# Performance work log

Hardware: AMD Instinct MI355X
Metric: run time of the kernel (lower is better)

Reference implementation:

```python
import jax, jax.numpy as jnp
import numpy as np

NUM_ENT = 50000
DIM = 128
NUM_REL = 1000  # num_rel * 2 (inverse relations)
E = 300000
SLOPE = 0.2      # args.leaky_relu_w
BN_EPS = 1e-5


def _leaky(x):
    return jax.nn.leaky_relu(x, SLOPE)


def _l2norm(x):
    n = jnp.linalg.norm(x, axis=-1, keepdims=True)
    return x / jnp.maximum(n, 1e-12)


def _batchnorm(x):
    # BatchNorm1d, training mode, fresh gamma=1/beta=0
    m = x.mean(axis=0)
    v = x.var(axis=0)
    return (x - m) / jnp.sqrt(v + BN_EPS)


def _propagate(i, j, etype, rel, x, watt, aatt, gcn, norm, num_ent):
    # gather -> relation-aware transform (opn='mult') -> attention -> scatter-add
    trans = x[j] * rel[etype]                       # [E, D]
    comb = jnp.concatenate([x[i], trans], axis=1)   # [E, 2D]
    score = (_leaky(comb @ watt) @ aatt)[:, 0]      # [E]
    # scatter softmax of attention score over destination nodes
    m = jax.ops.segment_max(score, i, num_segments=num_ent)
    m = jnp.where(jnp.isfinite(m), m, 0.0)
    e = jnp.exp(score - m[i])
    s = jax.ops.segment_sum(e, i, num_segments=num_ent)
    alpha = e / (s[i] + 1e-16)
    msg = (trans @ gcn) * alpha[:, None]
    if norm is not None:
        msg = msg * norm[:, None]
    return jax.ops.segment_sum(msg, i, num_segments=num_ent)


def _conv(ent, rel_in, edge_index, edge_type, w1, w2, gcn, loop_rel, watt, aatt):
    # RelationalAwareLayer.forward
    num_ent = ent.shape[0]
    rel = jnp.concatenate([rel_in, loop_rel], axis=0)
    rel = _leaky(rel @ w1) @ w2
    row, col = edge_index[0], edge_index[1]
    deg = jax.ops.segment_sum(jnp.ones((row.shape[0],), jnp.float32), row, num_segments=num_ent)
    dinv = jnp.where(deg > 0, deg ** -0.5, 0.0)
    norm = dinv[row]
    msg_n = _propagate(row, col, edge_type, rel, ent, watt, aatt, gcn, norm, num_ent)
    idx = jnp.arange(num_ent)
    loop_t = jnp.full((num_ent,), rel.shape[0] - 1)
    msg_s = _propagate(idx, idx, loop_t, rel, ent, watt, aatt, gcn, None, num_ent)
    return jnp.tanh(_batchnorm((msg_n + msg_s) / 2.0))


def setup_inputs() -> dict:
    key = jax.random.key(0)
    ks = jax.random.split(key, 24)
    g = lambda k, s: jax.random.normal(k, s, dtype=jnp.float32) * 0.05
    return {
        'edge_index': jax.random.randint(ks[0], (2, E), 0, NUM_ENT),
        'edge_type': jax.random.randint(ks[1], (E,), 0, NUM_REL),
        'ent_info_att': g(ks[2], (NUM_ENT, DIM)),
        'ent_completion_att': g(ks[3], (NUM_ENT, DIM)),
        'rel_completion_att': g(ks[4], (NUM_REL, DIM)),
        'rel_info_att': g(ks[5], (NUM_REL, DIM)),
        'align_linear1_1': g(ks[6], (2 * DIM, DIM)),
        'align_linear1_2': g(ks[7], (DIM, DIM)),
        'align_linear2_1': g(ks[8], (2 * DIM, DIM)),
        'align_linear2_2': g(ks[9], (DIM, DIM)),
        'rel_linear11': g(ks[10], (DIM, DIM)),
        'rel_linear12': g(ks[11], (DIM, DIM)),
        'rel_linear11_align': g(ks[12], (DIM, DIM)),
        'rel_linear12_align': g(ks[13], (DIM, DIM)),
        'all_linear_comp': g(ks[14], (3 * DIM, DIM)),
        # stacked per-layer conv params: [conv1_align, conv1_completion, conv2_align]
        'conv_w1': g(ks[15], (3, DIM, DIM)),
        'conv_w2': g(ks[16], (3, DIM, DIM)),
        'conv_gcn': g(ks[17], (3, DIM, DIM)),
        'conv_loop': g(ks[18], (3, 1, DIM)),
        'conv_watt': g(ks[19], (3, 2 * DIM, DIM)),
        'conv_aatt': g(ks[20], (3, DIM, 1)),
    }


def reference(edge_index, edge_type, ent_info_att, ent_completion_att,
              rel_completion_att, rel_info_att,
              align_linear1_1, align_linear1_2, align_linear2_1, align_linear2_2,
              rel_linear11, rel_linear12, rel_linear11_align, rel_linear12_align,
              all_linear_comp, conv_w1, conv_w2, conv_gcn, conv_loop, conv_watt, conv_aatt):
    # forward_base with num_gcn_layer == 2, dropout rate 0 (identity)
    init_comp = _l2norm(ent_completion_att)
    e1 = _leaky(jnp.concatenate([init_comp, ent_info_att], axis=1) @ align_linear1_1) @ align_linear1_2
    ao1 = _conv(e1, rel_info_att, edge_index, edge_type,
                conv_w1[0], conv_w2[0], conv_gcn[0], conv_loop[0], conv_watt[0], conv_aatt[0])
    co1 = _conv(ent_completion_att, rel_completion_att, edge_index, edge_type,
                conv_w1[1], conv_w2[1], conv_gcn[1], conv_loop[1], conv_watt[1], conv_aatt[1])
    pos1n = _l2norm(co1)
    e2 = _leaky(jnp.concatenate([pos1n, ao1], axis=1) @ align_linear2_1) @ align_linear2_2
    pr1 = _leaky(rel_completion_att @ rel_linear11) @ rel_linear12
    ari = _leaky(rel_info_att @ rel_linear11_align) @ rel_linear12_align
    ao2 = _conv(e2, ari, edge_index, edge_type,
                conv_w1[2], conv_w2[2], conv_gcn[2], conv_loop[2], conv_watt[2], conv_aatt[2])
    out = jnp.concatenate([e1, ao1, ao2], axis=1) @ all_linear_comp
    return (out, co1, pr1)
```

## Files before the change

### kernel.cpp

```cpp
#include <hip/hip_runtime.h>
#include <hip/hip_bf16.h>
#include <math.h>

#define D 128
#define DD 16384
#define NEMAX 96
typedef unsigned short u16;
typedef __attribute__((ext_vector_type(8))) short short8v;
typedef __attribute__((ext_vector_type(4))) short short4v;
typedef __attribute__((ext_vector_type(4))) float f32x4;

__device__ __forceinline__ u16 f2s(float v){
    union { __hip_bfloat16 h; u16 u; } c; c.h = __float2bfloat16(v); return c.u;
}
__device__ __forceinline__ float s2f(u16 u){
    union { __hip_bfloat16 h; u16 u; } c; c.u = u; return __bfloat162float(c.h);
}
__device__ __forceinline__ float lrelu(float x){ return x > 0.f ? x : 0.2f*x; }
__device__ __forceinline__ float ldx(const void* p, size_t i, int f32){
    return f32 ? ((const float*)p)[i] : s2f(((const u16*)p)[i]);
}

__global__ void k_zero(float* __restrict__ p, int n){
    for (int i = blockIdx.x*blockDim.x + threadIdx.x; i < n; i += gridDim.x*blockDim.x)
        p[i] = 0.f;
}
__global__ void k_filli(int* __restrict__ p, int v, int n){
    for (int i = blockIdx.x*blockDim.x + threadIdx.x; i < n; i += gridDim.x*blockDim.x)
        p[i] = v;
}
__global__ void k_f2b4(const float* __restrict__ in, u16* __restrict__ out, int n4){
    for (int i = blockIdx.x*blockDim.x + threadIdx.x; i < n4; i += gridDim.x*blockDim.x){
        float4 a = ((const float4*)in)[i];
        short4v pk;
        pk[0] = (short)f2s(a.x); pk[1] = (short)f2s(a.y);
        pk[2] = (short)f2s(a.z); pk[3] = (short)f2s(a.w);
        *(short4v*)(out + (size_t)i*4) = pk;
    }
}
__global__ void k_ideg(const int* __restrict__ row, int* __restrict__ deg, int E_){
    for (int i = blockIdx.x*blockDim.x + threadIdx.x; i < E_; i += gridDim.x*blockDim.x)
        atomicAdd(&deg[row[i]], 1);
}
__global__ void k_scan1(const int* __restrict__ ideg, int* __restrict__ rowptr,
                        int* __restrict__ bsum, int n){
    __shared__ int buf[256];
    int t = threadIdx.x, i = blockIdx.x*256 + t;
    int v = (i < n) ? ideg[i] : 0;
    buf[t] = v;
    __syncthreads();
    #pragma unroll
    for (int o = 1; o < 256; o <<= 1){
        int u = (t >= o) ? buf[t-o] : 0;
        __syncthreads();
        buf[t] += u;
        __syncthreads();
    }
    if (i < n) rowptr[i] = buf[t] - v;
    if (t == 255) bsum[blockIdx.x] = buf[255];
}
__global__ void k_scan2(int* __restrict__ bsum, int nb){
    __shared__ int buf[256];
    __shared__ int carry_s;
    int t = threadIdx.x;
    if (t == 0) carry_s = 0;
    __syncthreads();
    for (int base = 0; base < nb; base += 256){
        int v = (base + t < nb) ? bsum[base + t] : 0;
        buf[t] = v;
        __syncthreads();
        #pragma unroll
        for (int o = 1; o < 256; o <<= 1){
            int u = (t >= o) ? buf[t-o] : 0;
            __syncthreads();
            buf[t] += u;
            __syncthreads();
        }
        if (base + t < nb) bsum[base + t] = carry_s + buf[t] - v;
        int last = buf[255];
        __syncthreads();
        if (t == 0) carry_s += last;
        __syncthreads();
    }
}
__global__ void k_scan3(int* __restrict__ rowptr, const int* __restrict__ bsum,
                        int n, int E_){
    int i = blockIdx.x*blockDim.x + threadIdx.x;
    if (i < n) rowptr[i] += bsum[i >> 8];
    if (i == 0) rowptr[n] = E_;
}
__global__ void k_scatter(const int* __restrict__ row, const int* __restrict__ rowptr,
                          int* __restrict__ cnt, int* __restrict__ perm, int E_){
    for (int e = blockIdx.x*blockDim.x + threadIdx.x; e < E_; e += gridDim.x*blockDim.x){
        int i = row[e];
        int pos = rowptr[i] + atomicAdd(&cnt[i], 1);
        perm[pos] = e;
    }
}
__global__ void k_bmap(const int* __restrict__ rowptr, int* __restrict__ nstart,
                       int* __restrict__ nend, int n){
    for (int i = blockIdx.x*blockDim.x + threadIdx.x; i < n; i += gridDim.x*blockDim.x){
        int s = rowptr[i], e = rowptr[i+1];
        if (e > s){
            int b = s >> 6;
            atomicMin(&nstart[b], i);
            atomicMax(&nend[b], i);
        }
    }
}
template<bool F32>
__global__ void k_rsnorm(const void* __restrict__ x, float* __restrict__ rs){
    int r = blockIdx.x, t = threadIdx.x;
    __shared__ float sw[2];
    float v = ldx(x, (size_t)r*D + t, F32 ? 1 : 0);
    float s = v*v;
    #pragma unroll
    for (int o = 32; o > 0; o >>= 1) s += __shfl_xor(s, o, 64);
    if ((t & 63) == 0) sw[t >> 6] = s;
    __syncthreads();
    if (t == 0) rs[r] = 1.f / fmaxf(sqrtf(sw[0] + sw[1]), 1e-12f);
}
__global__ void k_rel_mlp(const float* __restrict__ src, const float* __restrict__ loopv, int R0,
                          const float* __restrict__ W1, const float* __restrict__ W2,
                          float* __restrict__ out){
    int r = blockIdx.x, t = threadIdx.x;
    __shared__ float v[D];
    __shared__ float h[D];
    v[t] = (r < R0) ? src[(size_t)r*D + t] : loopv[t];
    __syncthreads();
    float a = 0.f;
    #pragma unroll 8
    for (int k = 0; k < D; k++) a += v[k] * W1[(size_t)k*D + t];
    h[t] = lrelu(a);
    __syncthreads();
    float o = 0.f;
    #pragma unroll 8
    for (int k = 0; k < D; k++) o += h[k] * W2[(size_t)k*D + t];
    out[(size_t)r*D + t] = o;
}
__global__ void k_bnapply(const float* __restrict__ acc, const float* __restrict__ gp,
                          float inv_ne, int n, u16* __restrict__ dstb,
                          float* __restrict__ dstf){
    int d = threadIdx.x & 127;
    float m = gp[d] * inv_ne;
    float var = gp[128 + d] * inv_ne - m*m;
    float sc = rsqrtf(var + 1e-5f);
    for (int i = blockIdx.x*blockDim.x + threadIdx.x; i < n; i += gridDim.x*blockDim.x){
        float v = acc[i] * 0.5f;
        float r = tanhf((v - m) * sc);
        dstb[i] = f2s(r);
        if (dstf) dstf[i] = r;
    }
}

struct TEnt { const float* s; u16* d; int ldd; };
struct TTab { TEnt e[18]; };
__global__ void k_wprep(TTab tab){
    TEnt en = tab.e[blockIdx.x];
    int t = threadIdx.x;
    int n = t >> 1, h = t & 1;
    #pragma unroll
    for (int g = 0; g < 8; ++g){
        int k0 = h*64 + g*8;
        short8v pk;
        #pragma unroll
        for (int q = 0; q < 8; ++q) pk[q] = (short)f2s(en.s[(size_t)(k0+q)*D + n]);
        *(short8v*)(en.d + (size_t)n*en.ldd + k0) = pk;
    }
}

struct Srcs { const void* p0; const void* p1; const void* p2; int f0, f1, f2; };

template<int NSEG, int EPI>
__global__ __launch_bounds__(256) void k_mrow(Srcs S, const float* __restrict__ scale0,
        const u16* __restrict__ WT, void* __restrict__ out, int NE_,
        float* __restrict__ gp, u16* __restrict__ uout, const float* __restrict__ looprow){
    __shared__ __align__(16) short As[128*128];
    int tid = threadIdx.x;
    int row0 = blockIdx.x * 128;
    int lane = tid & 63, w = tid >> 6;
    int l15 = lane & 15, lq = lane >> 4;
    int nhalf = w & 1, mquad = w >> 1;
    f32x4 acc[4][4];
    #pragma unroll
    for (int a = 0; a < 4; a++)
        #pragma unroll
        for (int b = 0; b < 4; b++) acc[a][b] = (f32x4){0.f,0.f,0.f,0.f};

    int sr = tid >> 1, sh = tid & 1;
    int rr = row0 + sr; if (rr >= NE_) rr = NE_ - 1;

    #pragma unroll
    for (int s = 0; s < NSEG; ++s){
        const void* sp = (s == 0) ? S.p0 : (s == 1) ? S.p1 : S.p2;
        int sf = (s == 0) ? S.f0 : (s == 1) ? S.f1 : S.f2;
        float sc = (s == 0 && scale0) ? scale0[rr] : 1.f;
        if (s) __syncthreads();
        #pragma unroll
        for (int g = 0; g < 8; ++g){
            int k8 = sh*64 + g*8;
            short8v pk;
            if (sf){
                const float* fp = (const float*)sp + (size_t)rr*D + k8;
                #pragma unroll
                for (int q = 0; q < 8; ++q) pk[q] = (short)f2s(fp[q] * sc);
            } else {
                short8v sv = *(const short8v*)((const u16*)sp + (size_t)rr*D + k8);
                if (s == 0 && scale0){
                    #pragma unroll
                    for (int q = 0; q < 8; ++q) pk[q] = (short)f2s(s2f((u16)sv[q]) * sc);
                } else pk = sv;
            }
            *(short8v*)(As + sr*D + (((k8>>3) ^ (sr&7))<<3)) = pk;
        }
        __syncthreads();
        short8v bfr[4][4];
        #pragma unroll
        for (int nt = 0; nt < 4; ++nt)
            #pragma unroll
            for (int kk = 0; kk < 4; ++kk){
                size_t idx = (size_t)(nhalf*64 + nt*16 + l15)*(NSEG*D) + (size_t)s*D + kk*32 + lq*8;
                bfr[nt][kk] = *(const short8v*)(WT + idx);
            }
        #pragma unroll
        for (int mt = 0; mt < 4; ++mt){
            int ar = mquad*64 + mt*16 + l15;
            short8v afr[4];
            #pragma unroll
            for (int kk = 0; kk < 4; ++kk)
                afr[kk] = *(const short8v*)(As + ar*D + (((kk*4 + lq) ^ (ar&7))<<3));
            #pragma unroll
            for (int nt = 0; nt < 4; ++nt)
                #pragma unroll
                for (int kk = 0; kk < 4; ++kk)
                    acc[mt][nt] = __builtin_amdgcn_mfma_f32_16x16x32_bf16(
                        afr[kk], bfr[nt][kk], acc[mt][nt], 0, 0, 0);
        }
    }
    if (EPI == 3){
        float cs[4] = {0,0,0,0}, cs2[4] = {0,0,0,0};
        #pragma unroll
        for (int mt = 0; mt < 4; ++mt)
            #pragma unroll
            for (int nt = 0; nt < 4; ++nt)
                #pragma unroll
                for (int r = 0; r < 4; ++r){
                    int gr = row0 + mquad*64 + mt*16 + lq*4 + r;
                    if (gr >= NE_) continue;
                    int c = nhalf*64 + nt*16 + l15;
                    float v = acc[mt][nt][r];
                    ((float*)out)[(size_t)gr*D + c] = v;
                    float h = v * 0.5f;
                    cs[nt] += h; cs2[nt] += h*h;
                }
        __syncthreads();
        float* ps  = (float*)As;
        float* ps2 = ps + 1024;
        int slot = mquad*4 + lq;
        #pragma unroll
        for (int nt = 0; nt < 4; ++nt){
            int c = nhalf*64 + nt*16 + l15;
            ps[slot*128 + c]  = cs[nt];
            ps2[slot*128 + c] = cs2[nt];
        }
        __syncthreads();
        if (tid < 128){
            float s = 0.f, s2 = 0.f;
            #pragma unroll
            for (int q = 0; q < 8; ++q){ s += ps[q*128 + tid]; s2 += ps2[q*128 + tid]; }
            atomicAdd(&gp[tid], s);
            atomicAdd(&gp[128 + tid], s2);
        }
    } else {
        #pragma unroll
        for (int mt = 0; mt < 4; ++mt){
            #pragma unroll
            for (int nt = 0; nt < 4; ++nt){
                #pragma unroll
                for (int r = 0; r < 4; ++r){
                    int gr = row0 + mquad*64 + mt*16 + lq*4 + r;
                    if (gr >= NE_) continue;
                    int c = nhalf*64 + nt*16 + l15;
                    float v = acc[mt][nt][r];
                    if (EPI == 0) ((float*)out)[(size_t)gr*D + c] = v;
                    else ((u16*)out)[(size_t)gr*D + c] = f2s(EPI == 2 ? lrelu(v) : v);
                }
            }
        }
        if (EPI == 4){
            for (int idx = tid; idx < 128*128; idx += 256){
                int r2 = idx >> 7, c = idx & 127;
                int gr = row0 + r2;
                if (gr < NE_){
                    float v = s2f((u16)As[r2*D + ((((c>>3) ^ (r2&7))<<3) | (c&7))]) * looprow[c];
                    uout[(size_t)gr*D + c] = f2s(v);
                }
            }
        }
    }
}

__global__ __launch_bounds__(256) void k_fedge(
        const int* __restrict__ rowi, const int* __restrict__ coli, const int* __restrict__ ety,
        const int* __restrict__ rowptr, const int* __restrict__ perm,
        const int* __restrict__ nstart, const int* __restrict__ nend,
        const u16* __restrict__ x, const float* __restrict__ rel2,
        const u16* __restrict__ xattb, const u16* __restrict__ WT,
        const float* __restrict__ aatt, u16* __restrict__ u){
    __shared__ __align__(16) short As[NEMAX*D];
    __shared__ int jL[NEMAX], kL[NEMAX], iL[NEMAX];
    __shared__ float sc[NEMAX];
    __shared__ float red[2][NEMAX];
    int b = blockIdx.x;
    int ns = nstart[b];
    if (ns == 0x7fffffff) return;
    int nn = nend[b] - ns + 1;
    int tid = threadIdx.x;
    int estart = rowptr[ns];
    int ne = rowptr[ns + nn] - estart;
    if (ne > NEMAX) ne = NEMAX;
    int T = (ne + 15) >> 4;
    int nrows = T << 4;
    if (tid < ne){
        int e = perm[estart + tid];
        jL[tid] = coli[e]; kL[tid] = ety[e]; iL[tid] = rowi[e];
    }
    __syncthreads();
    for (int it = tid; it < nrows*4; it += 256){
        int p = it >> 2, part = it & 3;
        int ps = (p < ne) ? p : (ne - 1);
        int j = jL[ps], krel = kL[ps];
        #pragma unroll
        for (int g = 0; g < 4; ++g){
            int k8 = part*32 + g*8;
            short8v sv = *(const short8v*)(x + (size_t)j*D + k8);
            const float* rp = rel2 + (size_t)krel*D + k8;
            short8v pk;
            #pragma unroll
            for (int q = 0; q < 8; ++q) pk[q] = (short)f2s(s2f((u16)sv[q]) * rp[q]);
            *(short8v*)(As + p*D + (((k8>>3) ^ (p&7))<<3)) = pk;
        }
    }
    __syncthreads();
    int lane = tid & 63, w = tid >> 6;
    int l15 = lane & 15, lq = lane >> 4;
    int nhalf = w & 1, mq = w >> 1;
    short8v bfr[4][4];
    #pragma unroll
    for (int nt = 0; nt < 4; ++nt)
        #pragma unroll
        for (int kk = 0; kk < 4; ++kk)
            bfr[nt][kk] = *(const short8v*)(WT + (size_t)(nhalf*64 + nt*16 + l15)*D + kk*32 + lq*8);
    float av[4];
    #pragma unroll
    for (int nt = 0; nt < 4; ++nt) av[nt] = aatt[nhalf*64 + nt*16 + l15];

    for (int t = mq; t < T; t += 2){
        int ar = t*16 + l15;
        short8v afr[4];
        #pragma unroll
        for (int kk = 0; kk < 4; ++kk)
            afr[kk] = *(const short8v*)(As + ar*D + (((kk*4 + lq) ^ (ar&7))<<3));
        f32x4 acc[4];
        #pragma unroll
        for (int nt = 0; nt < 4; ++nt) acc[nt] = (f32x4){0.f,0.f,0.f,0.f};
        #pragma unroll
        for (int nt = 0; nt < 4; ++nt)
            #pragma unroll
            for (int kk = 0; kk < 4; ++kk)
                acc[nt] = __builtin_amdgcn_mfma_f32_16x16x32_bf16(
                    afr[kk], bfr[nt][kk], acc[nt], 0, 0, 0);
        #pragma unroll
        for (int r = 0; r < 4; ++r){
            int el = t*16 + lq*4 + r;
            float p = 0.f;
            if (el < ne){
                int ii = iL[el];
                #pragma unroll
                for (int nt = 0; nt < 4; ++nt){
                    float xv = s2f(xattb[(size_t)ii*D + nhalf*64 + nt*16 + l15]);
                    p += lrelu(acc[nt][r] + xv) * av[nt];
                }
            }
            p += __shfl_xor(p, 1, 64);
            p += __shfl_xor(p, 2, 64);
            p += __shfl_xor(p, 4, 64);
            p += __shfl_xor(p, 8, 64);
            if (l15 == 0 && el < NEMAX) red[nhalf][el] = p;
        }
    }
    __syncthreads();
    if (tid < ne) sc[tid] = expf(red[0][tid] + red[1][tid]);
    __syncthreads();
    if (tid < nn){
        int i = ns + tid;
        int s0 = rowptr[i] - estart, s1 = rowptr[i+1] - estart;
        if (s1 > NEMAX) s1 = NEMAX;
        if (s1 > s0){
            float sum = 0.f;
            for (int p = s0; p < s1; ++p) sum += sc[p];
            float coef = rsqrtf((float)(s1 - s0)) / (sum + 1e-16f);
            for (int p = s0; p < s1; ++p) sc[p] *= coef;
        }
    }
    __syncthreads();
    int c = tid & 127, nh = tid >> 7;
    for (int n = nh; n < nn; n += 2){
        int i = ns + n;
        int s0 = rowptr[i] - estart, s1 = rowptr[i+1] - estart;
        if (s1 > NEMAX) s1 = NEMAX;
        if (s1 <= s0) continue;
        float a = 0.f;
        for (int p = s0; p < s1; ++p)
            a += sc[p] * s2f((u16)As[p*D + ((((c>>3) ^ (p&7))<<3) | (c&7))]);
        size_t ad = (size_t)i*D + c;
        u[ad] = f2s(s2f(u[ad]) + a);
    }
}

extern "C" void kernel_launch(void* const* d_in, const int* in_sizes, int n_in,
                              void* d_out, int out_size, void* d_ws, size_t ws_size,
                              hipStream_t stream){
    const int* eidx = (const int*)d_in[0];
    const int* ety  = (const int*)d_in[1];
    const float* ent_info = (const float*)d_in[2];
    const float* ent_comp = (const float*)d_in[3];
    const float* rel_comp = (const float*)d_in[4];
    const float* rel_info = (const float*)d_in[5];
    const float* al11 = (const float*)d_in[6],  *al12 = (const float*)d_in[7];
    const float* al21 = (const float*)d_in[8],  *al22 = (const float*)d_in[9];
    const float* rl11 = (const float*)d_in[10], *rl12 = (const float*)d_in[11];
    const float* rl11a = (const float*)d_in[12], *rl12a = (const float*)d_in[13];
    const float* allw = (const float*)d_in[14];
    const float* cw1 = (const float*)d_in[15], *cw2 = (const float*)d_in[16];
    const float* cgcn = (const float*)d_in[17], *cloop = (const float*)d_in[18];
    const float* cwatt = (const float*)d_in[19], *caatt = (const float*)d_in[20];

    const int E  = in_sizes[1];
    const int NE = in_sizes[2] / D;
    const int NR = in_sizes[4] / D;
    const int* row = eidx;
    const int* col = eidx + E;
    const size_t NEd = (size_t)NE * D;
    float* outp = (float*)d_out;
    const int NB64 = (E + 63) / 64;

    char* wsb = (char*)d_ws;
    size_t off = 0;
    auto takeB = [&](size_t bytes) -> void* {
        void* q = wsb + off;
        off = (off + bytes + 255) & ~(size_t)255;
        return q;
    };
    float* accum = (float*)takeB(NEd * 4);
    u16*   hb    = (u16*)accum;
    u16*   xattb = (u16*) takeB(NEd * 2);
    u16*   ub    = (u16*) takeB(NEd * 2);
    u16*   e1b   = (u16*) takeB(NEd * 2);
    u16*   ao1b  = (u16*) takeB(NEd * 2);
    u16*   e2b   = (u16*) takeB(NEd * 2);
    u16*   cob   = (u16*) takeB(NEd * 2);
    float* rel2  = (float*)takeB((size_t)(NR+1)*D*4);
    float* ari   = (float*)takeB((size_t)NR*D*4);
    float* rs    = (float*)takeB((size_t)NE*4);
    int*   rowptr= (int*)  takeB((size_t)(NE+1)*4);
    int*   perm  = (int*)  takeB((size_t)E*4);
    int*   bsum  = (int*)  takeB(1024*4);
    int*   nstart= (int*)  takeB((size_t)NB64*4);
    int*   nend  = (int*)  takeB((size_t)NB64*4);
    int ZW = 2*NE + 768;
    int*   zz    = (int*)  takeB((size_t)ZW*4);
    int*   ideg  = zz;
    int*   cnt   = zz + NE;
    float* gp3   = (float*)(zz + 2*NE);
    u16*   wtXatt = (u16*)takeB((size_t)3*DD*2);
    u16*   wtScore= (u16*)takeB((size_t)3*DD*2);
    u16*   wtGcn  = (u16*)takeB((size_t)3*DD*2);
    u16*   wtAl11 = (u16*)takeB((size_t)2*DD*2);
    u16*   wtAl12 = (u16*)takeB((size_t)DD*2);
    u16*   wtAl21 = (u16*)takeB((size_t)2*DD*2);
    u16*   wtAl22 = (u16*)takeB((size_t)DD*2);
    u16*   wtAllw = (u16*)takeB((size_t)3*DD*2);
    u16*   xcb   = e2b;

    const int GS = 2048, BS = 256;
    const int RB = (NE + 127) / 128;
    const int NB = (NE + 255) / 256;
    const float inv_ne = 1.f / (float)NE;

    TTab tab;
    int ti = 0;
    for (int l = 0; l < 3; ++l){
        tab.e[ti++] = { cwatt + (size_t)l*2*DD,        wtXatt  + (size_t)l*DD, 128 };
        tab.e[ti++] = { cwatt + (size_t)l*2*DD + DD,   wtScore + (size_t)l*DD, 128 };
        tab.e[ti++] = { cgcn  + (size_t)l*DD,          wtGcn   + (size_t)l*DD, 128 };
    }
    tab.e[ti++] = { al11,       wtAl11,        256 };
    tab.e[ti++] = { al11 + DD,  wtAl11 + 128,  256 };
    tab.e[ti++] = { al12,       wtAl12,        128 };
    tab.e[ti++] = { al21,       wtAl21,        256 };
    tab.e[ti++] = { al21 + DD,  wtAl21 + 128,  256 };
    tab.e[ti++] = { al22,       wtAl22,        128 };
    tab.e[ti++] = { allw,            wtAllw,        384 };
    tab.e[ti++] = { allw + DD,       wtAllw + 128,  384 };
    tab.e[ti++] = { allw + 2*DD,     wtAllw + 256,  384 };
    k_wprep<<<18, 256, 0, stream>>>(tab);

    k_zero<<<256, BS, 0, stream>>>((float*)zz, ZW);
    k_filli<<<64, BS, 0, stream>>>(nstart, 0x7fffffff, NB64);
    k_filli<<<64, BS, 0, stream>>>(nend, -1, NB64);
    k_f2b4<<<GS, BS, 0, stream>>>(ent_comp, xcb, (int)(NEd/4));
    k_ideg<<<GS, BS, 0, stream>>>(row, ideg, E);
    k_scan1<<<NB, 256, 0, stream>>>(ideg, rowptr, bsum, NE);
    k_scan2<<<1, 256, 0, stream>>>(bsum, NB);
    k_scan3<<<NB, 256, 0, stream>>>(rowptr, bsum, NE, E);
    k_scatter<<<GS, BS, 0, stream>>>(row, rowptr, cnt, perm, E);
    k_bmap<<<NB, 256, 0, stream>>>(rowptr, nstart, nend, NE);

    k_rsnorm<true><<<NE, D, 0, stream>>>(ent_comp, rs);
    {
        Srcs S{ ent_comp, ent_info, nullptr, 1, 1, 0 };
        k_mrow<2, 2><<<RB, 256, 0, stream>>>(S, rs, wtAl11, hb, NE, nullptr, nullptr, nullptr);
        Srcs S2{ hb, nullptr, nullptr, 0, 0, 0 };
        k_mrow<1, 1><<<RB, 256, 0, stream>>>(S2, nullptr, wtAl12, e1b, NE, nullptr, nullptr, nullptr);
    }

    auto conv = [&](const u16* x, const float* relsrc, int l, u16* dstb, float* dstf){
        const float* w1   = cw1   + (size_t)l*DD;
        const float* w2   = cw2   + (size_t)l*DD;
        const float* aatt = caatt + (size_t)l*D;
        const float* lo   = cloop + (size_t)l*D;
        float* gp = gp3 + (size_t)l*256;
        k_rel_mlp<<<NR+1, D, 0, stream>>>(relsrc, lo, NR, w1, w2, rel2);
        Srcs Sx{ x, nullptr, nullptr, 0, 0, 0 };
        k_mrow<1, 4><<<RB, 256, 0, stream>>>(Sx, nullptr, wtXatt + (size_t)l*DD, xattb, NE,
                                             nullptr, ub, rel2 + (size_t)NR*D);
        k_fedge<<<NB64, 256, 0, stream>>>(row, col, ety, rowptr, perm, nstart, nend,
                                          x, rel2, xattb, wtScore + (size_t)l*DD, aatt, ub);
        Srcs Su{ ub, nullptr, nullptr, 0, 0, 0 };
        k_mrow<1, 3><<<RB, 256, 0, stream>>>(Su, nullptr, wtGcn + (size_t)l*DD, accum, NE,
                                             gp, nullptr, nullptr);
        k_bnapply<<<GS, BS, 0, stream>>>(accum, gp, inv_ne, (int)NEd, dstb, dstf);
    };

    conv(e1b, rel_info, 0, ao1b, nullptr);
    conv(xcb, rel_comp, 1, cob,  outp + NEd);

    k_rsnorm<false><<<NE, D, 0, stream>>>(cob, rs);
    {
        Srcs S{ cob, ao1b, nullptr, 0, 0, 0 };
        k_mrow<2, 2><<<RB, 256, 0, stream>>>(S, rs, wtAl21, hb, NE, nullptr, nullptr, nullptr);
        Srcs S2{ hb, nullptr, nullptr, 0, 0, 0 };
        k_mrow<1, 1><<<RB, 256, 0, stream>>>(S2, nullptr, wtAl22, e2b, NE, nullptr, nullptr, nullptr);
    }

    k_rel_mlp<<<NR, D, 0, stream>>>(rel_comp, nullptr, NR, rl11, rl12, outp + 2*NEd);
    k_rel_mlp<<<NR, D, 0, stream>>>(rel_info, nullptr, NR, rl11a, rl12a, ari);

    conv(e2b, ari, 2, cob, nullptr);

    {
        Srcs S{ e1b, ao1b, cob, 0, 0, 0 };
        k_mrow<3, 0><<<RB, 256, 0, stream>>>(S, nullptr, wtAllw, outp, NE, nullptr, nullptr, nullptr);
    }
}
```

Measured before the change: 747.5 us.

## Fuse relation MLPs, row-norm, and init kernels; tighten edge kernel staging

Merges all relation MLP passes (three conv layers plus pr1 and ari) into one kernel launch. Folds the L2 row normalisation into the GEMM's shared-memory tile, so the separate rsnorm kernels go away, and combines the zero/fill initialisation kernels into one. In the edge kernel it narrows the index arrays to 16-bit, batches the gathers of x, and adds an occupancy hint to launch_bounds. The goal is to cut launch overhead and extra passes over memory. The norm is now computed on bf16-rounded values, and 16-bit indices assume fewer than 65536 nodes and relations.

Result: slower. 789.5 us (+5.6%).

```diff
diff --git a/kernel.cpp b/kernel.cpp
--- a/kernel.cpp
+++ b/kernel.cpp
@@ -17,17 +17,13 @@
     union { __hip_bfloat16 h; u16 u; } c; c.u = u; return __bfloat162float(c.h);
 }
 __device__ __forceinline__ float lrelu(float x){ return x > 0.f ? x : 0.2f*x; }
-__device__ __forceinline__ float ldx(const void* p, size_t i, int f32){
-    return f32 ? ((const float*)p)[i] : s2f(((const u16*)p)[i]);
-}
-
-__global__ void k_zero(float* __restrict__ p, int n){
-    for (int i = blockIdx.x*blockDim.x + threadIdx.x; i < n; i += gridDim.x*blockDim.x)
-        p[i] = 0.f;
-}
-__global__ void k_filli(int* __restrict__ p, int v, int n){
-    for (int i = blockIdx.x*blockDim.x + threadIdx.x; i < n; i += gridDim.x*blockDim.x)
-        p[i] = v;
+
+__global__ void k_prepz(int* __restrict__ zz, int zw, int* __restrict__ nstart,
+                        int* __restrict__ nend, int nb){
+    int i = blockIdx.x*blockDim.x + threadIdx.x;
+    int stride = gridDim.x*blockDim.x;
+    for (int k = i; k < zw; k += stride) zz[k] = 0;
+    for (int k = i; k < nb; k += stride){ nstart[k] = 0x7fffffff; nend[k] = -1; }
 }
 __global__ void k_f2b4(const float* __restrict__ in, u16* __restrict__ out, int n4){
     for (int i = blockIdx.x*blockDim.x + threadIdx.x; i < n4; i += gridDim.x*blockDim.x){
@@ -107,36 +103,6 @@
             atomicMax(&nend[b], i);
         }
     }
-}
-template<bool F32>
-__global__ void k_rsnorm(const void* __restrict__ x, float* __restrict__ rs){
-    int r = blockIdx.x, t = threadIdx.x;
-    __shared__ float sw[2];
-    float v = ldx(x, (size_t)r*D + t, F32 ? 1 : 0);
-    float s = v*v;
-    #pragma unroll
-    for (int o = 32; o > 0; o >>= 1) s += __shfl_xor(s, o, 64);
-    if ((t & 63) == 0) sw[t >> 6] = s;
-    __syncthreads();
-    if (t == 0) rs[r] = 1.f / fmaxf(sqrtf(sw[0] + sw[1]), 1e-12f);
-}
-__global__ void k_rel_mlp(const float* __restrict__ src, const float* __restrict__ loopv, int R0,
-                          const float* __restrict__ W1, const float* __restrict__ W2,
-                          float* __restrict__ out){
-    int r = blockIdx.x, t = threadIdx.x;
-    __shared__ float v[D];
-    __shared__ float h[D];
-    v[t] = (r < R0) ? src[(size_t)r*D + t] : loopv[t];
-    __syncthreads();
-    float a = 0.f;
-    #pragma unroll 8
-    for (int k = 0; k < D; k++) a += v[k] * W1[(size_t)k*D + t];
-    h[t] = lrelu(a);
-    __syncthreads();
-    float o = 0.f;
-    #pragma unroll 8
-    for (int k = 0; k < D; k++) o += h[k] * W2[(size_t)k*D + t];
-    out[(size_t)r*D + t] = o;
 }
 __global__ void k_bnapply(const float* __restrict__ acc, const float* __restrict__ gp,
                           float inv_ne, int n, u16* __restrict__ dstb,
@@ -153,6 +119,62 @@
     }
 }
 
+__global__ void k_relprep(const float* __restrict__ rel_comp, const float* __restrict__ rel_info,
+        const float* __restrict__ rl11, const float* __restrict__ rl12,
+        const float* __restrict__ rl11a, const float* __restrict__ rl12a,
+        const float* __restrict__ cloop, const float* __restrict__ cw1,
+        const float* __restrict__ cw2, float* __restrict__ pr1out,
+        float* __restrict__ rel2all, int NR){
+    int b = blockIdx.x, t = threadIdx.x;
+    __shared__ float v[D];
+    __shared__ float h[D];
+    if (b < NR){
+        v[t] = rel_comp[(size_t)b*D + t];
+        __syncthreads();
+        float a = 0.f;
+        #pragma unroll 8
+        for (int k = 0; k < D; k++) a += v[k] * rl11[(size_t)k*D + t];
+        h[t] = lrelu(a);
+        __syncthreads();
+        float o = 0.f;
+        #pragma unroll 8
+        for (int k = 0; k < D; k++) o += h[k] * rl12[(size_t)k*D + t];
+        pr1out[(size_t)b*D + t] = o;
+        return;
+    }
+    int bb = b - NR;
+    int l = bb / (NR+1), r = bb - l*(NR+1);
+    float xv;
+    if (r == NR)      xv = cloop[l*D + t];
+    else if (l == 1)  xv = rel_comp[(size_t)r*D + t];
+    else              xv = rel_info[(size_t)r*D + t];
+    v[t] = xv;
+    __syncthreads();
+    if (l == 2 && r < NR){
+        float a = 0.f;
+        #pragma unroll 8
+        for (int k = 0; k < D; k++) a += v[k] * rl11a[(size_t)k*D + t];
+        h[t] = lrelu(a);
+        __syncthreads();
+        float o = 0.f;
+        #pragma unroll 8
+        for (int k = 0; k < D; k++) o += h[k] * rl12a[(size_t)k*D + t];
+        v[t] = o;
+        __syncthreads();
+    }
+    const float* w1 = cw1 + (size_t)l*DD;
+    const float* w2 = cw2 + (size_t)l*DD;
+    float a = 0.f;
+    #pragma unroll 8
+    for (int k = 0; k < D; k++) a += v[k] * w1[(size_t)k*D + t];
+    h[t] = lrelu(a);
+    __syncthreads();
+    float o = 0.f;
+    #pragma unroll 8
+    for (int k = 0; k < D; k++) o += h[k] * w2[(size_t)k*D + t];
+    rel2all[((size_t)l*(NR+1) + r)*D + t] = o;
+}
+
 struct TEnt { const float* s; u16* d; int ldd; };
 struct TTab { TEnt e[18]; };
 __global__ void k_wprep(TTab tab){
@@ -171,10 +193,10 @@
 
 struct Srcs { const void* p0; const void* p1; const void* p2; int f0, f1, f2; };
 
-template<int NSEG, int EPI>
-__global__ __launch_bounds__(256) void k_mrow(Srcs S, const float* __restrict__ scale0,
-        const u16* __restrict__ WT, void* __restrict__ out, int NE_,
-        float* __restrict__ gp, u16* __restrict__ uout, const float* __restrict__ looprow){
+template<int NSEG, int EPI, bool RSN>
+__global__ __launch_bounds__(256) void k_mrow(Srcs S, const u16* __restrict__ WT,
+        void* __restrict__ out, int NE_, float* __restrict__ gp,
+        u16* __restrict__ uout, const float* __restrict__ looprow){
     __shared__ __align__(16) short As[128*128];
     int tid = threadIdx.x;
     int row0 = blockIdx.x * 128;
@@ -194,7 +216,6 @@
     for (int s = 0; s < NSEG; ++s){
         const void* sp = (s == 0) ? S.p0 : (s == 1) ? S.p1 : S.p2;
         int sf = (s == 0) ? S.f0 : (s == 1) ? S.f1 : S.f2;
-        float sc = (s == 0 && scale0) ? scale0[rr] : 1.f;
         if (s) __syncthreads();
         #pragma unroll
         for (int g = 0; g < 8; ++g){
@@ -203,15 +224,33 @@
             if (sf){
                 const float* fp = (const float*)sp + (size_t)rr*D + k8;
                 #pragma unroll
-                for (int q = 0; q < 8; ++q) pk[q] = (short)f2s(fp[q] * sc);
+                for (int q = 0; q < 8; ++q) pk[q] = (short)f2s(fp[q]);
             } else {
-                short8v sv = *(const short8v*)((const u16*)sp + (size_t)rr*D + k8);
-                if (s == 0 && scale0){
-                    #pragma unroll
-                    for (int q = 0; q < 8; ++q) pk[q] = (short)f2s(s2f((u16)sv[q]) * sc);
-                } else pk = sv;
+                pk = *(const short8v*)((const u16*)sp + (size_t)rr*D + k8);
             }
             *(short8v*)(As + sr*D + (((k8>>3) ^ (sr&7))<<3)) = pk;
+        }
+        if (RSN && s == 0){
+            float ss = 0.f;
+            #pragma unroll
+            for (int g = 0; g < 8; ++g){
+                int k8 = sh*64 + g*8;
+                short8v v = *(const short8v*)(As + sr*D + (((k8>>3) ^ (sr&7))<<3));
+                #pragma unroll
+                for (int q = 0; q < 8; ++q){ float f = s2f((u16)v[q]); ss += f*f; }
+            }
+            ss += __shfl_xor(ss, 1, 64);
+            float rsc = 1.f / fmaxf(sqrtf(ss), 1e-12f);
+            #pragma unroll
+            for (int g = 0; g < 8; ++g){
+                int k8 = sh*64 + g*8;
+                short* ap = As + sr*D + (((k8>>3) ^ (sr&7))<<3);
+                short8v v = *(const short8v*)ap;
+                short8v pk;
+                #pragma unroll
+                for (int q = 0; q < 8; ++q) pk[q] = (short)f2s(s2f((u16)v[q]) * rsc);
+                *(short8v*)ap = pk;
+            }
         }
         __syncthreads();
         short8v bfr[4][4];
@@ -300,7 +339,7 @@
     }
 }
 
-__global__ __launch_bounds__(256) void k_fedge(
+__global__ __launch_bounds__(256, 6) void k_fedge(
         const int* __restrict__ rowi, const int* __restrict__ coli, const int* __restrict__ ety,
         const int* __restrict__ rowptr, const int* __restrict__ perm,
         const int* __restrict__ nstart, const int* __restrict__ nend,
@@ -308,7 +347,7 @@
         const u16* __restrict__ xattb, const u16* __restrict__ WT,
         const float* __restrict__ aatt, u16* __restrict__ u){
     __shared__ __align__(16) short As[NEMAX*D];
-    __shared__ int jL[NEMAX], kL[NEMAX], iL[NEMAX];
+    __shared__ u16 jL[NEMAX], kL[NEMAX], iL[NEMAX];
     __shared__ float sc[NEMAX];
     __shared__ float red[2][NEMAX];
     int b = blockIdx.x;
@@ -323,22 +362,29 @@
     int nrows = T << 4;
     if (tid < ne){
         int e = perm[estart + tid];
-        jL[tid] = coli[e]; kL[tid] = ety[e]; iL[tid] = rowi[e];
-    }
-    __syncthreads();
-    for (int it = tid; it < nrows*4; it += 256){
-        int p = it >> 2, part = it & 3;
-        int ps = (p < ne) ? p : (ne - 1);
-        int j = jL[ps], krel = kL[ps];
-        #pragma unroll
-        for (int g = 0; g < 4; ++g){
-            int k8 = part*32 + g*8;
-            short8v sv = *(const short8v*)(x + (size_t)j*D + k8);
-            const float* rp = rel2 + (size_t)krel*D + k8;
-            short8v pk;
-            #pragma unroll
-            for (int q = 0; q < 8; ++q) pk[q] = (short)f2s(s2f((u16)sv[q]) * rp[q]);
-            *(short8v*)(As + p*D + (((k8>>3) ^ (p&7))<<3)) = pk;
+        jL[tid] = (u16)coli[e]; kL[tid] = (u16)ety[e]; iL[tid] = (u16)rowi[e];
+    }
+    __syncthreads();
+    int nU = nrows * 4;
+    #pragma unroll
+    for (int hf = 0; hf < 2; ++hf){
+        int uidx = tid + hf*256;
+        if (uidx < nU){
+            int p = uidx >> 2, part = uidx & 3;
+            int ps = (p < ne) ? p : (ne - 1);
+            int j = jL[ps], krel = kL[ps];
+            const u16* xp = x + (size_t)j*D + part*32;
+            short8v xv[4];
+            #pragma unroll
+            for (int g = 0; g < 4; ++g) xv[g] = *(const short8v*)(xp + g*8);
+            const float* rp = rel2 + (size_t)krel*D + part*32;
+            #pragma unroll
+            for (int g = 0; g < 4; ++g){
+                short8v pk;
+                #pragma unroll
+                for (int q = 0; q < 8; ++q) pk[q] = (short)f2s(s2f((u16)xv[g][q]) * rp[g*8+q]);
+                *(short8v*)(As + p*D + (((part*4 + g) ^ (p&7))<<3)) = pk;
+            }
         }
     }
     __syncthreads();
@@ -378,8 +424,8 @@
                 int ii = iL[el];
                 #pragma unroll
                 for (int nt = 0; nt < 4; ++nt){
-                    float xv = s2f(xattb[(size_t)ii*D + nhalf*64 + nt*16 + l15]);
-                    p += lrelu(acc[nt][r] + xv) * av[nt];
+                    float xv2 = s2f(xattb[(size_t)ii*D + nhalf*64 + nt*16 + l15]);
+                    p += lrelu(acc[nt][r] + xv2) * av[nt];
                 }
             }
             p += __shfl_xor(p, 1, 64);
@@ -460,9 +506,7 @@
     u16*   ao1b  = (u16*) takeB(NEd * 2);
     u16*   e2b   = (u16*) takeB(NEd * 2);
     u16*   cob   = (u16*) takeB(NEd * 2);
-    float* rel2  = (float*)takeB((size_t)(NR+1)*D*4);
-    float* ari   = (float*)takeB((size_t)NR*D*4);
-    float* rs    = (float*)takeB((size_t)NE*4);
+    float* rel2all = (float*)takeB((size_t)3*(NR+1)*D*4);
     int*   rowptr= (int*)  takeB((size_t)(NE+1)*4);
     int*   perm  = (int*)  takeB((size_t)E*4);
     int*   bsum  = (int*)  takeB(1024*4);
@@ -506,9 +550,7 @@
     tab.e[ti++] = { allw + 2*DD,     wtAllw + 256,  384 };
     k_wprep<<<18, 256, 0, stream>>>(tab);
 
-    k_zero<<<256, BS, 0, stream>>>((float*)zz, ZW);
-    k_filli<<<64, BS, 0, stream>>>(nstart, 0x7fffffff, NB64);
-    k_filli<<<64, BS, 0, stream>>>(nend, -1, NB64);
+    k_prepz<<<256, BS, 0, stream>>>(zz, ZW, nstart, nend, NB64);
     k_f2b4<<<GS, BS, 0, stream>>>(ent_comp, xcb, (int)(NEd/4));
     k_ideg<<<GS, BS, 0, stream>>>(row, ideg, E);
     k_scan1<<<NB, 256, 0, stream>>>(ideg, rowptr, bsum, NE);
@@ -517,50 +559,46 @@
     k_scatter<<<GS, BS, 0, stream>>>(row, rowptr, cnt, perm, E);
     k_bmap<<<NB, 256, 0, stream>>>(rowptr, nstart, nend, NE);
 
-    k_rsnorm<true><<<NE, D, 0, stream>>>(ent_comp, rs);
+    k_relprep<<<NR + 3*(NR+1), D, 0, stream>>>(rel_comp, rel_info, rl11, rl12,
+                                               rl11a, rl12a, cloop, cw1, cw2,
+                                               outp + 2*NEd, rel2all, NR);
+
     {
         Srcs S{ ent_comp, ent_info, nullptr, 1, 1, 0 };
-        k_mrow<2, 2><<<RB, 256, 0, stream>>>(S, rs, wtAl11, hb, NE, nullptr, nullptr, nullptr);
+        k_mrow<2, 2, true><<<RB, 256, 0, stream>>>(S, wtAl11, hb, NE, nullptr, nullptr, nullptr);
         Srcs S2{ hb, nullptr, nullptr, 0, 0, 0 };
-        k_mrow<1, 1><<<RB, 256, 0, stream>>>(S2, nullptr, wtAl12, e1b, NE, nullptr, nullptr, nullptr);
-    }
-
-    auto conv = [&](const u16* x, const float* relsrc, int l, u16* dstb, float* dstf){
-        const float* w1   = cw1   + (size_t)l*DD;
-        const float* w2   = cw2   + (size_t)l*DD;
-        const float* aatt = caatt + (size_t)l*D;
-        const float* lo   = cloop + (size_t)l*D;
+        k_mrow<1, 1, false><<<RB, 256, 0, stream>>>(S2, wtAl12, e1b, NE, nullptr, nullptr, nullptr);
+    }
+
+    auto conv = [&](const u16* x, int l, u16* dstb, float* dstf){
+        const float* aatt  = caatt + (size_t)l*D;
+        const float* rel2l = rel2all + (size_t)l*(NR+1)*D;
         float* gp = gp3 + (size_t)l*256;
-        k_rel_mlp<<<NR+1, D, 0, stream>>>(relsrc, lo, NR, w1, w2, rel2);
         Srcs Sx{ x, nullptr, nullptr, 0, 0, 0 };
-        k_mrow<1, 4><<<RB, 256, 0, stream>>>(Sx, nullptr, wtXatt + (size_t)l*DD, xattb, NE,
-                                             nullptr, ub, rel2 + (size_t)NR*D);
+        k_mrow<1, 4, false><<<RB, 256, 0, stream>>>(Sx, wtXatt + (size_t)l*DD, xattb, NE,
+                                                    nullptr, ub, rel2l + (size_t)NR*D);
         k_fedge<<<NB64, 256, 0, stream>>>(row, col, ety, rowptr, perm, nstart, nend,
-                                          x, rel2, xattb, wtScore + (size_t)l*DD, aatt, ub);
+                                          x, rel2l, xattb, wtScore + (size_t)l*DD, aatt, ub);
         Srcs Su{ ub, nullptr, nullptr, 0, 0, 0 };
-        k_mrow<1, 3><<<RB, 256, 0, stream>>>(Su, nullptr, wtGcn + (size_t)l*DD, accum, NE,
-                                             gp, nullptr, nullptr);
+        k_mrow<1, 3, false><<<RB, 256, 0, stream>>>(Su, wtGcn + (size_t)l*DD, accum, NE,
+                                                    gp, nullptr, nullptr);
         k_bnapply<<<GS, BS, 0, stream>>>(accum, gp, inv_ne, (int)NEd, dstb, dstf);
     };
 
-    conv(e1b, rel_info, 0, ao1b, nullptr);
-    conv(xcb, rel_comp, 1, cob,  outp + NEd);
-
-    k_rsnorm<false><<<NE, D, 0, stream>>>(cob, rs);
+    conv(e1b, 0, ao1b, nullptr);
+    conv(xcb, 1, cob,  outp + NEd);
+
     {
         Srcs S{ cob, ao1b, nullptr, 0, 0, 0 };
-        k_mrow<2, 2><<<RB, 256, 0, stream>>>(S, rs, wtAl21, hb, NE, nullptr, nullptr, nullptr);
+        k_mrow<2, 2, true><<<RB, 256, 0, stream>>>(S, wtAl21, hb, NE, nullptr, nullptr, nullptr);
         Srcs S2{ hb, nullptr, nullptr, 0, 0, 0 };
-        k_mrow<1, 1><<<RB, 256, 0, stream>>>(S2, nullptr, wtAl22, e2b, NE, nullptr, nullptr, nullptr);
-    }
-
-    k_rel_mlp<<<NR, D, 0, stream>>>(rel_comp, nullptr, NR, rl11, rl12, outp + 2*NEd);
-    k_rel_mlp<<<NR, D, 0, stream>>>(rel_info, nullptr, NR, rl11a, rl12a, ari);
-
-    conv(e2b, ari, 2, cob, nullptr);
+        k_mrow<1, 1, false><<<RB, 256, 0, stream>>>(S2, wtAl22, e2b, NE, nullptr, nullptr, nullptr);
+    }
+
+    conv(e2b, 2, cob, nullptr);
 
     {
         Srcs S{ e1b, ao1b, cob, 0, 0, 0 };
-        k_mrow<3, 0><<<RB, 256, 0, stream>>>(S, nullptr, wtAllw, outp, NE, nullptr, nullptr, nullptr);
-    }
-}
+        k_mrow<3, 0, false><<<RB, 256, 0, stream>>>(S, wtAllw, outp, NE, nullptr, nullptr, nullptr);
+    }
+}
```
